# Performance work log

Hardware: AMD Instinct MI355X
Metric: run time of the kernel (lower is better)

## Reference

```python
import jax, jax.numpy as jnp
import numpy as np

NUM_TOKENS = 8192
HIDDEN = 4096
TOTAL_EXPERTS = 512
TOP_K = 12
ROUTED_SCALING_FACTOR = 2.5


def setup_inputs() -> dict:
    key = jax.random.key(0)
    k1, k2, k3 = jax.random.split(key, 3)
    hidden_states = jax.random.normal(k1, (NUM_TOKENS, HIDDEN), dtype=jnp.float32)
    # HF layout: classifier.weight is [total_experts, hidden_size]
    classifier_weight = jax.random.normal(k2, (TOTAL_EXPERTS, HIDDEN), dtype=jnp.float32) * (HIDDEN ** -0.5)
    e_score_correction_bias = jax.random.normal(k3, (TOTAL_EXPERTS,), dtype=jnp.float32) * 0.02
    return {
        "hidden_states": hidden_states,
        "classifier_weight": classifier_weight,
        "e_score_correction_bias": e_score_correction_bias,
    }


def reference(hidden_states, classifier_weight, e_score_correction_bias):
    # Linear (no bias): [T, H] @ [H, E] -> [T, E]
    router_logits = jnp.einsum("th,eh->te", hidden_states, classifier_weight)
    router_probs = jax.nn.softmax(router_logits, axis=-1)
    # Bias only affects expert SELECTION, not the routing weights.
    biased = router_probs + e_score_correction_bias  # [T, E]
    _, selected_experts = jax.lax.top_k(biased, TOP_K)  # [T, K] int32
    # Gather original (unbiased) probs at the selected experts.
    routing_weights = jnp.take_along_axis(router_probs, selected_experts, axis=-1)  # [T, K]
    routing_weights = routing_weights * jnp.float32(ROUTED_SCALING_FACTOR)
    return routing_weights, selected_experts
```

## Files before the change

kernel.cpp:

```cpp
#include <hip/hip_runtime.h>
#include <math.h>

#define T_TOKENS 8192
#define HID      4096
#define NEXP     512
#define TOPK     12
#define RSCALE   2.5f


__device__ __forceinline__ unsigned int fkey(float f) {
    unsigned int u = __float_as_uint(f);
    return (u & 0x80000000u) ? ~u : (u | 0x80000000u);
}

__device__ __forceinline__ float pick8(const float* p, int j) {
    float v = p[0];
    if (j == 1) v = p[1];
    if (j == 2) v = p[2];
    if (j == 3) v = p[3];
    if (j == 4) v = p[4];
    if (j == 5) v = p[5];
    if (j == 6) v = p[6];
    if (j == 7) v = p[7];
    return v;
}


typedef __attribute__((ext_vector_type(8))) _Float16 f16x8;
typedef __attribute__((ext_vector_type(4))) float    f32x4;

#define BM   128
#define BM2  64
#define BN   128
#define BKF  32
#define ROWB 144

__device__ __forceinline__ void cvt4(const float4 f, uint2& h, uint2& l) {
    _Float16 h0 = (_Float16)f.x, h1 = (_Float16)f.y;
    _Float16 h2 = (_Float16)f.z, h3 = (_Float16)f.w;
    float r0 = (f.x - (float)h0) * 4096.f;
    float r1 = (f.y - (float)h1) * 4096.f;
    float r2 = (f.z - (float)h2) * 4096.f;
    float r3 = (f.w - (float)h3) * 4096.f;
    _Float16 l0 = (_Float16)r0, l1 = (_Float16)r1;
    _Float16 l2 = (_Float16)r2, l3 = (_Float16)r3;
    union P { _Float16 q[2]; unsigned int u; } p;
    p.q[0] = h0; p.q[1] = h1; h.x = p.u;
    p.q[0] = h2; p.q[1] = h3; h.y = p.u;
    p.q[0] = l0; p.q[1] = l1; l.x = p.u;
    p.q[0] = l2; p.q[1] = l3; l.y = p.u;
}

__device__ __forceinline__ void load_lds16(const void* g, void* l) {
    __builtin_amdgcn_global_load_lds((const __attribute__((address_space(1))) void*)g,
                                     (__attribute__((address_space(3))) void*)l,
                                     16, 0, 0);
}


__global__ void wconv_kernel(const float* __restrict__ W, uint4* __restrict__ Wp) {
    const int gid = blockIdx.x * 256 + threadIdx.x;
    const int e  = gid >> 10;
    const int kc = (gid >> 3) & 127;
    const int p  = gid & 7;
    const int g  = p ^ (e & 7);
    const int kbase = kc * 32 + (g & 3) * 8;
    const float* src = W + (size_t)e * HID + kbase;
    const float4 f0 = *(const float4*)src;
    const float4 f1 = *(const float4*)(src + 4);
    const float v[8] = {f0.x, f0.y, f0.z, f0.w, f1.x, f1.y, f1.z, f1.w};

    union H { _Float16 f; unsigned short u; } cv;
    unsigned short h[8];
    if (g < 4) {
        #pragma unroll
        for (int j = 0; j < 8; j++) { cv.f = (_Float16)(v[j] * 64.f); h[j] = cv.u; }
    } else {
        #pragma unroll
        for (int j = 0; j < 8; j++) {
            const float w64 = v[j] * 64.f;
            const _Float16 hh = (_Float16)w64;
            cv.f = (_Float16)((w64 - (float)hh) * 4096.f);
            h[j] = cv.u;
        }
    }
    union O { unsigned short q[8]; uint4 u; } o;
    #pragma unroll
    for (int j = 0; j < 8; j++) o.q[j] = h[j];
    Wp[(size_t)(kc * 512 + e) * 8 + p] = o.u;
}


__launch_bounds__(256, 2)
__global__ void gemm2_kernel(const float* __restrict__ X,
                             const uint4* __restrict__ Wp,
                             float* __restrict__ logits)
{
    __shared__ __align__(16) unsigned char Xs[BM2 * ROWB];
    __shared__ __align__(16) unsigned char Ws[BN * 128];

    const int tid  = threadIdx.x;
    const int lane = tid & 63;
    const int wave = tid >> 6;

    const int x8    = blockIdx.x & 7;
    const int i64   = blockIdx.x >> 3;
    const int n_grp = x8 >> 1;
    const int m_grp = i64 * 2 + (x8 & 1);
    const int tok0  = m_grp * BM2;
    const int e0    = n_grp * BN;

    const int waveM = (wave >> 1) * 32;
    const int waveN = (wave & 1) * 64;
    const int m16   = lane & 15;
    const int q     = lane >> 4;

    const float* Xb = X + (size_t)tok0 * HID;

    const char* wsrc = (const char*)Wp + (size_t)(e0 + wave * 32) * 128 + lane * 16;
    unsigned char* wdst = Ws + (wave * 32) * 128;

    float4 px[2];
    #pragma unroll
    for (int s = 0; s < 2; s++) {
        const int flat = s * 256 + tid;
        const int row = flat >> 3, grp = flat & 7;
        px[s] = *(const float4*)&Xb[(size_t)row * HID + grp * 4];
    }

    f32x4 accH[2][4], accC[2][4];
    #pragma unroll
    for (int mi = 0; mi < 2; mi++)
        #pragma unroll
        for (int ni = 0; ni < 4; ni++) { accH[mi][ni] = (f32x4)0.f; accC[mi][ni] = (f32x4)0.f; }

    #pragma unroll 1
    for (int kc = 0; kc < HID / BKF; kc++) {
        __syncthreads();

        #pragma unroll
        for (int s = 0; s < 4; s++)
            load_lds16(wsrc + (size_t)kc * (512 * 128) + s * 1024, wdst + s * 1024);

        #pragma unroll
        for (int s = 0; s < 2; s++) {
            const int flat = s * 256 + tid;
            const int row = flat >> 3, grp = flat & 7;
            uint2 h, l;
            cvt4(px[s], h, l);
            *(uint2*)(Xs + row * ROWB + grp * 8)      = h;
            *(uint2*)(Xs + row * ROWB + 80 + grp * 8) = l;
        }
        __syncthreads();

        if (kc + 1 < HID / BKF) {
            #pragma unroll
            for (int s = 0; s < 2; s++) {
                const int flat = s * 256 + tid;
                const int row = flat >> 3, grp = flat & 7;
                px[s] = *(const float4*)&Xb[(size_t)row * HID + (kc + 1) * BKF + grp * 4];
            }
        }

        f16x8 Ah[2], Al[2], Bh[4], Bl[4];
        #pragma unroll
        for (int mi = 0; mi < 2; mi++) {
            const unsigned char* p = Xs + (waveM + mi * 16 + m16) * ROWB + q * 16;
            Ah[mi] = *(const f16x8*)p;
            Al[mi] = *(const f16x8*)(p + 80);
        }
        #pragma unroll
        for (int ni = 0; ni < 4; ni++) {
            const int row = waveN + ni * 16 + m16;
            const unsigned char* pr = Ws + row * 128;
            const int r7 = row & 7;
            Bh[ni] = *(const f16x8*)(pr + ((q ^ r7) * 16));
            Bl[ni] = *(const f16x8*)(pr + (((4 | q) ^ r7) * 16));
        }

        #pragma unroll
        for (int mi = 0; mi < 2; mi++)
            #pragma unroll
            for (int ni = 0; ni < 4; ni++) {
                accH[mi][ni] = __builtin_amdgcn_mfma_f32_16x16x32_f16(Ah[mi], Bh[ni], accH[mi][ni], 0, 0, 0);
                accC[mi][ni] = __builtin_amdgcn_mfma_f32_16x16x32_f16(Ah[mi], Bl[ni], accC[mi][ni], 0, 0, 0);
                accC[mi][ni] = __builtin_amdgcn_mfma_f32_16x16x32_f16(Al[mi], Bh[ni], accC[mi][ni], 0, 0, 0);
            }
    }

    #pragma unroll
    for (int mi = 0; mi < 2; mi++)
        #pragma unroll
        for (int ni = 0; ni < 4; ni++) {
            const int e = e0 + waveN + ni * 16 + m16;
            #pragma unroll
            for (int r = 0; r < 4; r++) {
                const int token = tok0 + waveM + mi * 16 + q * 4 + r;
                logits[(size_t)token * NEXP + e] =
                    (accH[mi][ni][r] + accC[mi][ni][r] * (1.f / 4096.f)) * (1.f / 64.f);
            }
        }
}


__launch_bounds__(256, 1)
__global__ void gemm_kernel(const float* __restrict__ X,
                            const float* __restrict__ W,
                            float* __restrict__ logits)
{
    __shared__ __align__(16) unsigned char Xs[BM * ROWB];
    __shared__ __align__(16) unsigned char Ws[BN * ROWB];

    const int tid  = threadIdx.x;
    const int lane = tid & 63;
    const int wave = tid >> 6;

    const int n_grp = blockIdx.x & 3;
    const int m_grp = blockIdx.x >> 2;
    const int tok0  = m_grp * BM;
    const int e0    = n_grp * BN;

    const int waveM = (wave >> 1) * 64;
    const int waveN = (wave & 1) * 64;
    const int m16   = lane & 15;
    const int q     = lane >> 4;

    const float* Xb = X + (size_t)tok0 * HID;
    const float* Wb = W + (size_t)e0 * HID;

    float4 px[4], pw[4];
    #pragma unroll
    for (int s = 0; s < 4; s++) {
        const int flat = s * 256 + tid;
        const int row = flat >> 3, grp = flat & 7;
        px[s] = *(const float4*)&Xb[(size_t)row * HID + grp * 4];
        pw[s] = *(const float4*)&Wb[(size_t)row * HID + grp * 4];
    }

    f32x4 accH[4][4], accC[4][4];
    #pragma unroll
    for (int mi = 0; mi < 4; mi++)
        #pragma unroll
        for (int ni = 0; ni < 4; ni++) { accH[mi][ni] = (f32x4)0.f; accC[mi][ni] = (f32x4)0.f; }

    #pragma unroll 1
    for (int k0 = 0; k0 < HID; k0 += BKF) {
        #pragma unroll
        for (int s = 0; s < 4; s++) {
            const int flat = s * 256 + tid;
            const int row = flat >> 3, grp = flat & 7;
            uint2 h, l;
            cvt4(px[s], h, l);
            *(uint2*)(Xs + row * ROWB + grp * 8)      = h;
            *(uint2*)(Xs + row * ROWB + 80 + grp * 8) = l;
            const float4 w64 = make_float4(pw[s].x * 64.f, pw[s].y * 64.f,
                                           pw[s].z * 64.f, pw[s].w * 64.f);
            cvt4(w64, h, l);
            *(uint2*)(Ws + row * ROWB + grp * 8)      = h;
            *(uint2*)(Ws + row * ROWB + 80 + grp * 8) = l;
        }
        __syncthreads();

        if (k0 + BKF < HID) {
            #pragma unroll
            for (int s = 0; s < 4; s++) {
                const int flat = s * 256 + tid;
                const int row = flat >> 3, grp = flat & 7;
                px[s] = *(const float4*)&Xb[(size_t)row * HID + (k0 + BKF) + grp * 4];
                pw[s] = *(const float4*)&Wb[(size_t)row * HID + (k0 + BKF) + grp * 4];
            }
        }

        f16x8 Ah[4], Al[4], Bh[4], Bl[4];
        #pragma unroll
        for (int mi = 0; mi < 4; mi++) {
            const unsigned char* p = Xs + (waveM + mi * 16 + m16) * ROWB + q * 16;
            Ah[mi] = *(const f16x8*)p;
            Al[mi] = *(const f16x8*)(p + 80);
        }
        #pragma unroll
        for (int ni = 0; ni < 4; ni++) {
            const unsigned char* p = Ws + (waveN + ni * 16 + m16) * ROWB + q * 16;
            Bh[ni] = *(const f16x8*)p;
            Bl[ni] = *(const f16x8*)(p + 80);
        }

        #pragma unroll
        for (int mi = 0; mi < 4; mi++)
            #pragma unroll
            for (int ni = 0; ni < 4; ni++) {
                accH[mi][ni] = __builtin_amdgcn_mfma_f32_16x16x32_f16(Ah[mi], Bh[ni], accH[mi][ni], 0, 0, 0);
                accC[mi][ni] = __builtin_amdgcn_mfma_f32_16x16x32_f16(Ah[mi], Bl[ni], accC[mi][ni], 0, 0, 0);
                accC[mi][ni] = __builtin_amdgcn_mfma_f32_16x16x32_f16(Al[mi], Bh[ni], accC[mi][ni], 0, 0, 0);
            }
        __syncthreads();
    }

    #pragma unroll
    for (int mi = 0; mi < 4; mi++)
        #pragma unroll
        for (int ni = 0; ni < 4; ni++) {
            const int e = e0 + waveN + ni * 16 + m16;
            #pragma unroll
            for (int r = 0; r < 4; r++) {
                const int token = tok0 + waveM + mi * 16 + q * 4 + r;
                logits[(size_t)token * NEXP + e] =
                    (accH[mi][ni][r] + accC[mi][ni][r] * (1.f / 4096.f)) * (1.f / 64.f);
            }
        }
}


__launch_bounds__(256, 4)
__global__ void topk_kernel(const float* __restrict__ logits,
                            const float* __restrict__ bias,
                            float* __restrict__ out)
{
    const int lane = threadIdx.x & 63;
    const int wave = threadIdx.x >> 6;
    const int tok  = blockIdx.x * 4 + wave;

    const float4 bs0 = *(const float4*)&bias[4 * lane];
    const float4 bs1 = *(const float4*)&bias[256 + 4 * lane];
    const float br[8] = {bs0.x, bs0.y, bs0.z, bs0.w, bs1.x, bs1.y, bs1.z, bs1.w};

    const float4 z0 = *(const float4*)&logits[(size_t)tok * NEXP + 4 * lane];
    const float4 z1 = *(const float4*)&logits[(size_t)tok * NEXP + 256 + 4 * lane];
    float z[8] = {z0.x, z0.y, z0.z, z0.w, z1.x, z1.y, z1.z, z1.w};

    float m = z[0];
    #pragma unroll
    for (int j = 1; j < 8; j++) m = fmaxf(m, z[j]);
    #pragma unroll
    for (int off = 32; off >= 1; off >>= 1) m = fmaxf(m, __shfl_xor(m, off));

    float p[8];
    float s = 0.f;
    #pragma unroll
    for (int j = 0; j < 8; j++) { p[j] = expf(z[j] - m); s += p[j]; }
    #pragma unroll
    for (int off = 32; off >= 1; off >>= 1) s += __shfl_xor(s, off);
    const float inv = 1.f / s;

    float pb[8];
    unsigned long long kj[8];
    #pragma unroll
    for (int j = 0; j < 8; j++) {
        pb[j] = p[j] * inv;
        const int e = (j < 4) ? (4 * lane + j) : (256 + 4 * lane + (j - 4));
        kj[j] = ((unsigned long long)fkey(pb[j] + br[j]) << 32) |
                (unsigned long long)(unsigned int)(1023 - e);
    }
    unsigned long long lk = kj[0];
    #pragma unroll
    for (int j = 1; j < 8; j++) lk = (kj[j] > lk) ? kj[j] : lk;

    for (int kk = 0; kk < TOPK; kk++) {
        unsigned long long key = lk;
        #pragma unroll
        for (int off = 32; off >= 1; off >>= 1) {
            unsigned long long o = __shfl_xor(key, off);
            key = (o > key) ? o : key;
        }
        const int estar = 1023 - (int)(unsigned int)(key & 0xffffffffull);

        int lstar, jstar;
        if (estar < 256) { lstar = estar >> 2;         jstar = estar & 3; }
        else             { lstar = (estar - 256) >> 2; jstar = 4 + ((estar - 256) & 3); }

        const float pj   = pick8(pb, jstar);
        const float psel = __shfl(pj, lstar);

        if (lane == lstar) {
            if (jstar == 0) kj[0] = 0ull;
            if (jstar == 1) kj[1] = 0ull;
            if (jstar == 2) kj[2] = 0ull;
            if (jstar == 3) kj[3] = 0ull;
            if (jstar == 4) kj[4] = 0ull;
            if (jstar == 5) kj[5] = 0ull;
            if (jstar == 6) kj[6] = 0ull;
            if (jstar == 7) kj[7] = 0ull;
            unsigned long long nl = kj[0];
            #pragma unroll
            for (int j = 1; j < 8; j++) nl = (kj[j] > nl) ? kj[j] : nl;
            lk = nl;
        }

        if (lane == 0) {
            out[(size_t)tok * TOPK + kk] = psel * RSCALE;
            out[(size_t)T_TOKENS * TOPK + (size_t)tok * TOPK + kk] = (float)estar;
        }
    }
}


#define TM   32
#define BK   16
#define EPAD (NEXP + 4)
#define XPAD 36

__launch_bounds__(256, 1)
__global__ void router_kernel(const float* __restrict__ X,
                              const float* __restrict__ W,
                              const float* __restrict__ bias,
                              float* __restrict__ out)
{
    __shared__ float Wsh[BK][EPAD];
    __shared__ float Xsh[BK][XPAD];

    const int tid  = threadIdx.x;
    const int lane = tid & 63;
    const int wave = tid >> 6;
    const int tok0 = blockIdx.x * TM;

    float acc[8][8];
    #pragma unroll
    for (int i = 0; i < 8; i++)
        #pragma unroll
        for (int j = 0; j < 8; j++) acc[i][j] = 0.f;

    const int xt = tid >> 4;
    const int xk = tid & 15;

    for (int k0 = 0; k0 < HID; k0 += BK) {
        #pragma unroll
        for (int r = 0; r < 2; r++) {
            int t = r * 16 + xt;
            Xsh[xk][t] = X[(size_t)(tok0 + t) * HID + k0 + xk];
        }
        #pragma unroll
        for (int r = 0; r < 8; r++) {
            int flat4 = r * 256 + tid;
            int e  = flat4 >> 2;
            int kq = (flat4 & 3) * 4;
            const float4 wv = *(const float4*)&W[(size_t)e * HID + k0 + kq];
            Wsh[kq + 0][e] = wv.x;
            Wsh[kq + 1][e] = wv.y;
            Wsh[kq + 2][e] = wv.z;
            Wsh[kq + 3][e] = wv.w;
        }
        __syncthreads();

        #pragma unroll
        for (int k = 0; k < BK; k++) {
            float4 b0 = *(const float4*)&Wsh[k][4 * lane];
            float4 b1 = *(const float4*)&Wsh[k][256 + 4 * lane];
            float4 a0 = *(const float4*)&Xsh[k][wave * 8];
            float4 a1 = *(const float4*)&Xsh[k][wave * 8 + 4];
            float a[8] = {a0.x, a0.y, a0.z, a0.w, a1.x, a1.y, a1.z, a1.w};
            float b[8] = {b0.x, b0.y, b0.z, b0.w, b1.x, b1.y, b1.z, b1.w};
            #pragma unroll
            for (int i = 0; i < 8; i++)
                #pragma unroll
                for (int j = 0; j < 8; j++)
                    acc[i][j] = fmaf(a[i], b[j], acc[i][j]);
        }
        __syncthreads();
    }

    const float4 bs0 = *(const float4*)&bias[4 * lane];
    const float4 bs1 = *(const float4*)&bias[256 + 4 * lane];
    const float br[8] = {bs0.x, bs0.y, bs0.z, bs0.w, bs1.x, bs1.y, bs1.z, bs1.w};

    for (int i = 0; i < 8; i++) {
        const int tok = tok0 + wave * 8 + i;

        float m = acc[i][0];
        #pragma unroll
        for (int j = 1; j < 8; j++) m = fmaxf(m, acc[i][j]);
        #pragma unroll
        for (int off = 32; off >= 1; off >>= 1) m = fmaxf(m, __shfl_xor(m, off));

        float p[8];
        float s = 0.f;
        #pragma unroll
        for (int j = 0; j < 8; j++) { p[j] = expf(acc[i][j] - m); s += p[j]; }
        #pragma unroll
        for (int off = 32; off >= 1; off >>= 1) s += __shfl_xor(s, off);
        const float inv = 1.f / s;

        float pb[8], bb[8];
        #pragma unroll
        for (int j = 0; j < 8; j++) {
            pb[j] = p[j] * inv;
            bb[j] = pb[j] + br[j];
        }

        for (int kk = 0; kk < TOPK; kk++) {
            unsigned long long key = 0ull;
            #pragma unroll
            for (int j = 0; j < 8; j++) {
                int e = (j < 4) ? (4 * lane + j) : (256 + 4 * lane + (j - 4));
                unsigned long long k64 =
                    ((unsigned long long)fkey(bb[j]) << 32) |
                    (unsigned long long)(unsigned int)(1023 - e);
                key = (k64 > key) ? k64 : key;
            }
            #pragma unroll
            for (int off = 32; off >= 1; off >>= 1) {
                unsigned long long o = __shfl_xor(key, off);
                key = (o > key) ? o : key;
            }
            const int estar = 1023 - (int)(unsigned int)(key & 0xffffffffull);

            int lstar, jstar;
            if (estar < 256) { lstar = estar >> 2;         jstar = estar & 3; }
            else             { lstar = (estar - 256) >> 2; jstar = 4 + ((estar - 256) & 3); }

            const float pj   = pick8(pb, jstar);
            const float psel = __shfl(pj, lstar);

            if (lane == lstar) {
                if (jstar == 0) bb[0] = -INFINITY;
                if (jstar == 1) bb[1] = -INFINITY;
                if (jstar == 2) bb[2] = -INFINITY;
                if (jstar == 3) bb[3] = -INFINITY;
                if (jstar == 4) bb[4] = -INFINITY;
                if (jstar == 5) bb[5] = -INFINITY;
                if (jstar == 6) bb[6] = -INFINITY;
                if (jstar == 7) bb[7] = -INFINITY;
            }

            if (lane == 0) {
                out[(size_t)tok * TOPK + kk] = psel * RSCALE;
                out[(size_t)T_TOKENS * TOPK + (size_t)tok * TOPK + kk] = (float)estar;
            }
        }
    }
}


extern "C" void kernel_launch(void* const* d_in, const int* in_sizes, int n_in,
                              void* d_out, int out_size, void* d_ws, size_t ws_size,
                              hipStream_t stream)
{
    const float* X    = (const float*)d_in[0];
    const float* W    = (const float*)d_in[1];
    const float* bias = (const float*)d_in[2];
    float* out = (float*)d_out;

    const size_t logits_bytes = (size_t)T_TOKENS * NEXP * sizeof(float);
    const size_t wp_bytes     = (size_t)NEXP * HID * 4;

    if (ws_size >= logits_bytes + wp_bytes) {
        float* logits = (float*)d_ws;
        uint4* Wp     = (uint4*)((char*)d_ws + logits_bytes);
        wconv_kernel<<<dim3(2048), dim3(256), 0, stream>>>(W, Wp);
        gemm2_kernel<<<dim3(512), dim3(256), 0, stream>>>(X, Wp, logits);
        topk_kernel<<<dim3(T_TOKENS / 4), dim3(256), 0, stream>>>(logits, bias, out);
    } else if (ws_size >= logits_bytes) {
        float* logits = (float*)d_ws;
        gemm_kernel<<<dim3(256), dim3(256), 0, stream>>>(X, W, logits);
        topk_kernel<<<dim3(T_TOKENS / 4), dim3(256), 0, stream>>>(logits, bias, out);
    } else {
        router_kernel<<<dim3(T_TOKENS / TM), dim3(256), 0, stream>>>(X, W, bias, out);
    }
}
```

Measured before the change: 380.8 us.

## Process two K-slices per barrier pair and remap block-to-tile ordering

The GEMM main loop now stages two 32-wide K-slices of X and W into LDS per iteration, which halves the number of __syncthreads pairs and doubles the loads in flight. The block index mapping also changes so that consecutive blocks share token rows across the four expert groups, which is meant to improve L2 reuse of X. In exchange, LDS use and prefetch registers double, which may reduce occupancy at the 2-blocks-per-CU launch bound.

```diff
diff --git a/kernel.cpp b/kernel.cpp
--- a/kernel.cpp
+++ b/kernel.cpp
@@ -96,8 +96,8 @@
                              const uint4* __restrict__ Wp,
                              float* __restrict__ logits)
 {
-    __shared__ __align__(16) unsigned char Xs[BM2 * ROWB];
-    __shared__ __align__(16) unsigned char Ws[BN * 128];
+    __shared__ __align__(16) unsigned char Xs[2][BM2 * ROWB];
+    __shared__ __align__(16) unsigned char Ws[2][BN * 128];
 
     const int tid  = threadIdx.x;
     const int lane = tid & 63;
@@ -105,8 +105,8 @@
 
     const int x8    = blockIdx.x & 7;
     const int i64   = blockIdx.x >> 3;
-    const int n_grp = x8 >> 1;
-    const int m_grp = i64 * 2 + (x8 & 1);
+    const int m_grp = x8 * 16 + (i64 >> 2);
+    const int n_grp = i64 & 3;
     const int tok0  = m_grp * BM2;
     const int e0    = n_grp * BN;
 
@@ -118,14 +118,16 @@
     const float* Xb = X + (size_t)tok0 * HID;
 
     const char* wsrc = (const char*)Wp + (size_t)(e0 + wave * 32) * 128 + lane * 16;
-    unsigned char* wdst = Ws + (wave * 32) * 128;
-
-    float4 px[2];
-    #pragma unroll
-    for (int s = 0; s < 2; s++) {
-        const int flat = s * 256 + tid;
-        const int row = flat >> 3, grp = flat & 7;
-        px[s] = *(const float4*)&Xb[(size_t)row * HID + grp * 4];
+    const int   wofs = (wave * 32) * 128;
+
+    const int xrow = tid >> 3;
+    const int xgrp = tid & 7;
+
+    float4 px[4];
+    #pragma unroll
+    for (int s = 0; s < 4; s++) {
+        const int row = (s & 1) * 32 + xrow;
+        px[s] = *(const float4*)&Xb[(size_t)row * HID + (s >> 1) * BKF + xgrp * 4];
     }
 
     f32x4 accH[2][4], accC[2][4];
@@ -135,57 +137,60 @@
         for (int ni = 0; ni < 4; ni++) { accH[mi][ni] = (f32x4)0.f; accC[mi][ni] = (f32x4)0.f; }
 
     #pragma unroll 1
-    for (int kc = 0; kc < HID / BKF; kc++) {
+    for (int j = 0; j < 64; j++) {
         __syncthreads();
 
         #pragma unroll
-        for (int s = 0; s < 4; s++)
-            load_lds16(wsrc + (size_t)kc * (512 * 128) + s * 1024, wdst + s * 1024);
-
-        #pragma unroll
-        for (int s = 0; s < 2; s++) {
-            const int flat = s * 256 + tid;
-            const int row = flat >> 3, grp = flat & 7;
+        for (int sl = 0; sl < 2; sl++)
+            #pragma unroll
+            for (int s = 0; s < 4; s++)
+                load_lds16(wsrc + (size_t)(2 * j + sl) * (512 * 128) + s * 1024,
+                           &Ws[sl][wofs + s * 1024]);
+
+        #pragma unroll
+        for (int s = 0; s < 4; s++) {
+            const int row = (s & 1) * 32 + xrow;
             uint2 h, l;
             cvt4(px[s], h, l);
-            *(uint2*)(Xs + row * ROWB + grp * 8)      = h;
-            *(uint2*)(Xs + row * ROWB + 80 + grp * 8) = l;
+            *(uint2*)(&Xs[s >> 1][row * ROWB + xgrp * 8])      = h;
+            *(uint2*)(&Xs[s >> 1][row * ROWB + 80 + xgrp * 8]) = l;
         }
         __syncthreads();
 
-        if (kc + 1 < HID / BKF) {
-            #pragma unroll
-            for (int s = 0; s < 2; s++) {
-                const int flat = s * 256 + tid;
-                const int row = flat >> 3, grp = flat & 7;
-                px[s] = *(const float4*)&Xb[(size_t)row * HID + (kc + 1) * BKF + grp * 4];
-            }
-        }
-
-        f16x8 Ah[2], Al[2], Bh[4], Bl[4];
-        #pragma unroll
-        for (int mi = 0; mi < 2; mi++) {
-            const unsigned char* p = Xs + (waveM + mi * 16 + m16) * ROWB + q * 16;
-            Ah[mi] = *(const f16x8*)p;
-            Al[mi] = *(const f16x8*)(p + 80);
-        }
-        #pragma unroll
-        for (int ni = 0; ni < 4; ni++) {
-            const int row = waveN + ni * 16 + m16;
-            const unsigned char* pr = Ws + row * 128;
-            const int r7 = row & 7;
-            Bh[ni] = *(const f16x8*)(pr + ((q ^ r7) * 16));
-            Bl[ni] = *(const f16x8*)(pr + (((4 | q) ^ r7) * 16));
-        }
-
-        #pragma unroll
-        for (int mi = 0; mi < 2; mi++)
+        if (j + 1 < 64) {
+            #pragma unroll
+            for (int s = 0; s < 4; s++) {
+                const int row = (s & 1) * 32 + xrow;
+                px[s] = *(const float4*)&Xb[(size_t)row * HID + (j + 1) * 64 + (s >> 1) * BKF + xgrp * 4];
+            }
+        }
+
+        #pragma unroll
+        for (int sl = 0; sl < 2; sl++) {
+            f16x8 Ah[2], Al[2], Bh[4], Bl[4];
+            #pragma unroll
+            for (int mi = 0; mi < 2; mi++) {
+                const unsigned char* p = &Xs[sl][(waveM + mi * 16 + m16) * ROWB + q * 16];
+                Ah[mi] = *(const f16x8*)p;
+                Al[mi] = *(const f16x8*)(p + 80);
+            }
             #pragma unroll
             for (int ni = 0; ni < 4; ni++) {
-                accH[mi][ni] = __builtin_amdgcn_mfma_f32_16x16x32_f16(Ah[mi], Bh[ni], accH[mi][ni], 0, 0, 0);
-                accC[mi][ni] = __builtin_amdgcn_mfma_f32_16x16x32_f16(Ah[mi], Bl[ni], accC[mi][ni], 0, 0, 0);
-                accC[mi][ni] = __builtin_amdgcn_mfma_f32_16x16x32_f16(Al[mi], Bh[ni], accC[mi][ni], 0, 0, 0);
-            }
+                const int row = waveN + ni * 16 + m16;
+                const unsigned char* pr = &Ws[sl][row * 128];
+                const int r7 = row & 7;
+                Bh[ni] = *(const f16x8*)(pr + ((q ^ r7) * 16));
+                Bl[ni] = *(const f16x8*)(pr + (((4 | q) ^ r7) * 16));
+            }
+            #pragma unroll
+            for (int mi = 0; mi < 2; mi++)
+                #pragma unroll
+                for (int ni = 0; ni < 4; ni++) {
+                    accH[mi][ni] = __builtin_amdgcn_mfma_f32_16x16x32_f16(Ah[mi], Bh[ni], accH[mi][ni], 0, 0, 0);
+                    accC[mi][ni] = __builtin_amdgcn_mfma_f32_16x16x32_f16(Ah[mi], Bl[ni], accC[mi][ni], 0, 0, 0);
+                    accC[mi][ni] = __builtin_amdgcn_mfma_f32_16x16x32_f16(Al[mi], Bh[ni], accC[mi][ni], 0, 0, 0);
+                }
+        }
     }
 
     #pragma unroll
```

Measured after the change: 315.0 us, median of 2. 17.3% less time.
